# Kernel optimization log

Measured on AMD Instinct MI355X. Metric: run time of the kernel, lower is better.

The kernel has to match this reference:

```python
import jax, jax.numpy as jnp
import numpy as np

N_NODES = 50000
N_EDGES = 800000
N_GRAPHS = 64
IN_DIM = 128
HID = 64
HEADS = 4
LAT = 32
BN_EPS = 1e-5


def setup_inputs() -> dict:
    key = jax.random.key(0)
    ks = jax.random.split(key, 16)
    x = jax.random.normal(ks[0], (N_NODES, IN_DIM), jnp.float32)
    edge_index = jax.random.randint(ks[1], (2, N_EDGES), 0, N_NODES, dtype=jnp.int64)
    batch = jnp.sort(jax.random.randint(ks[2], (N_NODES,), 0, N_GRAPHS, dtype=jnp.int64))

    def lin(k, fan_in, shape):
        return (jax.random.normal(k, shape, jnp.float32) / np.sqrt(fan_in)).astype(jnp.float32)

    d = {"x": x, "edge_index": edge_index, "batch": batch}
    dims = [IN_DIM, HID, HID]
    i = 3
    for l, din in enumerate(dims):
        d[f"Wl{l}"] = lin(ks[i], din, (din, HEADS * HID)); i += 1
        d[f"Wr{l}"] = lin(ks[i], din, (din, HEADS * HID)); i += 1
        d[f"att{l}"] = lin(ks[i], HID, (HEADS, HID)); i += 1
        d[f"b{l}"] = jnp.zeros((HID,), jnp.float32)
    d["bn_gamma"] = jnp.ones((HID,), jnp.float32)
    d["bn_beta"] = jnp.zeros((HID,), jnp.float32)
    d["fc_W"] = lin(ks[i], HID, (LAT, HID)); i += 1
    d["fc_b"] = jnp.zeros((LAT,), jnp.float32)
    return d


def _gatv2_conv(x, Wl, Wr, att, b, src, dst):
    # PyG GATv2Conv, concat=False: mean over heads. src -> dst message flow.
    n = x.shape[0]
    H, D = att.shape
    xl = (x @ Wl).reshape(n, H, D)   # source-side transform
    xr = (x @ Wr).reshape(n, H, D)   # target-side transform
    e = jax.nn.leaky_relu(xl[src] + xr[dst], 0.2)        # [E, H, D]
    logits = jnp.einsum('ehd,hd->eh', e, att)            # [E, H]
    # segment softmax over incoming edges of each dst node
    m = jax.ops.segment_max(logits, dst, num_segments=n)
    p = jnp.exp(logits - m[dst])
    denom = jax.ops.segment_sum(p, dst, num_segments=n)
    alpha = p / (denom[dst] + 1e-16)                     # [E, H]
    out = jax.ops.segment_sum(alpha[..., None] * xl[src], dst, num_segments=n)  # [N, H, D]
    return out.mean(axis=1) + b


def reference(x, edge_index, batch, Wl0, Wr0, att0, b0, Wl1, Wr1, att1, b1,
              Wl2, Wr2, att2, b2, bn_gamma, bn_beta, fc_W, fc_b):
    src, dst = edge_index[0], edge_index[1]
    h = x
    for (Wl, Wr, att, b) in ((Wl0, Wr0, att0, b0), (Wl1, Wr1, att1, b1), (Wl2, Wr2, att2, b2)):
        h = _gatv2_conv(h, Wl, Wr, att, b, src, dst)
        h = jax.nn.leaky_relu(h, 0.1)
        # dropout omitted (deterministic reference / eval semantics)
    pooled = jax.ops.segment_sum(h, batch, num_segments=N_GRAPHS)  # [G, HID]
    mean = pooled.mean(axis=0)
    var = pooled.var(axis=0)  # biased variance, matches BN training normalization
    y = (pooled - mean) / jnp.sqrt(var + BN_EPS) * bn_gamma + bn_beta
    return y @ fc_W.T + fc_b
```

## Files before the change

kernel.cpp:

```cpp
#include <hip/hip_runtime.h>
#include <hip/hip_bf16.h>
#include <math.h>
#include <string.h>

#define N_NODES 50000
#define N_EDGES 800000
#define N_GRAPHS 64
#define IN_DIM 128
#define HID 64
#define HEADS 4
#define LAT 32
#define SCAN_BLOCKS ((N_NODES + 255) / 256)
#define ES_CAP 960000

typedef __attribute__((ext_vector_type(8))) short bf16x8;
typedef __attribute__((ext_vector_type(4))) float floatx4;
typedef __attribute__((ext_vector_type(2))) float f32x2;

__device__ inline unsigned short f2bf(float f) {
    unsigned u = __float_as_uint(f);
    return (unsigned short)((u + 0x7fffu + ((u >> 16) & 1u)) >> 16);
}

__device__ inline unsigned pkbf(float x, float y) {
    float2 f{x, y};
    __hip_bfloat162 h = __float22bfloat162_rn(f);
    unsigned u;
    memcpy(&u, &h, sizeof(u));
    return u;
}

__device__ inline f32x2 bfpair(unsigned u) {
    f32x2 r;
    r.x = __uint_as_float(u << 16);
    r.y = __uint_as_float(u & 0xffff0000u);
    return r;
}

__device__ inline float rowsum16(float x) {
    x += __int_as_float(__builtin_amdgcn_mov_dpp(__float_as_int(x), 0x128, 0xf, 0xf, false));
    x += __int_as_float(__builtin_amdgcn_mov_dpp(__float_as_int(x), 0x124, 0xf, 0xf, false));
    x += __int_as_float(__builtin_amdgcn_mov_dpp(__float_as_int(x), 0x122, 0xf, 0xf, false));
    x += __int_as_float(__builtin_amdgcn_mov_dpp(__float_as_int(x), 0x121, 0xf, 0xf, false));
    return x;
}

__global__ __launch_bounds__(256) void prep_kernel(
    const float* __restrict__ x, unsigned* __restrict__ xbf,
    const float* __restrict__ Wl0, const float* __restrict__ Wr0,
    const float* __restrict__ Wl1, const float* __restrict__ Wr1,
    const float* __restrict__ Wl2, const float* __restrict__ Wr2,
    unsigned short* __restrict__ B0, unsigned short* __restrict__ B1,
    unsigned short* __restrict__ B2,
    int* __restrict__ cnt, float* __restrict__ pooled, int* __restrict__ done,
    uint4* __restrict__ es4) {
    int b = blockIdx.x, t = threadIdx.x;
    if (b < 3072) {
        for (int i = b * 256 + t; i < N_NODES * IN_DIM / 2; i += 3072 * 256) {
            float2 v = reinterpret_cast<const float2*>(x)[i];
            xbf[i] = pkbf(v.x, v.y);
        }
    } else if (b < 3584) {
        int idx = (b - 3072) * 256 + t;
        const float *Wl, *Wr;
        unsigned short* B;
        int KC, local;
        if (idx < 65536)      { Wl = Wl0; Wr = Wr0; B = B0; KC = 4; local = idx; }
        else if (idx < 98304) { Wl = Wl1; Wr = Wr1; B = B1; KC = 2; local = idx - 65536; }
        else                  { Wl = Wl2; Wr = Wr2; B = B2; KC = 2; local = idx - 98304; }
        int j = local & 7;
        int lane = (local >> 3) & 63;
        int rem = local >> 9;
        int kc = rem % KC;
        int tile = rem / KC;
        int k = kc * 32 + (lane >> 4) * 8 + j;
        int tt = tile & 15;
        int n = (tt >> 2) * 64 + (lane & 15) * 4 + (tt & 3);
        const float* W = (tile < 16) ? Wl : Wr;
        B[local] = f2bf(W[k * 256 + n]);
    } else if (b < 3840) {
        int idx = (b - 3584) * 256 + t;
        if (idx < N_NODES) cnt[idx] = 0;
        if (idx < N_GRAPHS * HID) pooled[idx] = 0.f;
        if (idx == 0) *done = 0;
    } else {
        int idx = (b - 3840) * 256 + t;
        for (int i = idx; i < ES_CAP / 4; i += 65536)
            es4[i] = uint4{0, 0, 0, 0};
    }
}

__global__ __launch_bounds__(256) void deg_kernel(const int4* __restrict__ dsts4,
                                                  int* __restrict__ cnt, int E4) {
    int i = blockIdx.x * 256 + threadIdx.x;
    if (i < E4) {
        int4 d = dsts4[i];
        atomicAdd(&cnt[d.x], 1);
        atomicAdd(&cnt[d.y], 1);
        atomicAdd(&cnt[d.z], 1);
        atomicAdd(&cnt[d.w], 1);
    }
}

__global__ __launch_bounds__(256) void scan_kernel(const int* __restrict__ cnt,
                                                   int* __restrict__ offs,
                                                   int* __restrict__ sc,
                                                   int* __restrict__ agg) {
    __shared__ int buf[256];
    int b = blockIdx.x, t = threadIdx.x;
    int i = b * 256 + t;
    int v = (i < N_NODES) ? ((cnt[i] + 3) & ~3) : 0;
    buf[t] = v;
    __syncthreads();
    #pragma unroll
    for (int off = 1; off < 256; off <<= 1) {
        int tmp = (t >= off) ? buf[t - off] : 0;
        __syncthreads();
        buf[t] += tmp;
        __syncthreads();
    }
    int incl = buf[t];
    if (t == 255)
        __hip_atomic_store(&agg[b], buf[255] | 0x40000000,
                           __ATOMIC_RELEASE, __HIP_MEMORY_SCOPE_AGENT);
    int contrib = 0;
    if (t < b) {
        int vv;
        do {
            vv = __hip_atomic_load(&agg[t], __ATOMIC_ACQUIRE, __HIP_MEMORY_SCOPE_AGENT);
        } while (vv < 0 || !(vv & 0x40000000));
        contrib = vv & 0x3FFFFFFF;
    }
    __syncthreads();
    buf[t] = contrib;
    __syncthreads();
    for (int off = 128; off; off >>= 1) {
        if (t < off) buf[t] += buf[t + off];
        __syncthreads();
    }
    if (i < N_NODES) {
        offs[i] = buf[0] + incl - v;
        sc[i] = 0;
    }
}

__global__ __launch_bounds__(256) void scatter_kernel(const int4* __restrict__ srcs4,
                                                      const int4* __restrict__ dsts4,
                                                      const int* __restrict__ offs,
                                                      int* __restrict__ sc,
                                                      int* __restrict__ es, int E4) {
    int i = blockIdx.x * 256 + threadIdx.x;
    if (i < E4) {
        int4 s = srcs4[i];
        int4 d = dsts4[i];
        es[offs[d.x] + atomicAdd(&sc[d.x], 1)] = s.x;
        es[offs[d.y] + atomicAdd(&sc[d.y], 1)] = s.y;
        es[offs[d.z] + atomicAdd(&sc[d.z], 1)] = s.z;
        es[offs[d.w] + atomicAdd(&sc[d.w], 1)] = s.w;
    }
}

template <int K>
__global__ __launch_bounds__(512) void gemm_mfma_kernel(
    const unsigned short* __restrict__ Abf,
    const unsigned short* __restrict__ Bpk,
    unsigned* __restrict__ xlp_u,
    unsigned* __restrict__ xrp_u) {
    constexpr int KC = K / 32;
    constexpr int CHUNKS = 64 * K / 8;
    __shared__ short As[CHUNKS * 8];
    int br = blockIdx.x * 64;
    int t = threadIdx.x;

    for (int c = t; c < CHUNKS; c += 512) {
        int rt = c / (KC * 64);
        int rem = c % (KC * 64);
        int kc = rem >> 6;
        int quad = (rem >> 4) & 3, l16 = rem & 15;
        int row = br + rt * 16 + l16;
        if (row >= N_NODES) row = N_NODES - 1;
        *reinterpret_cast<uint4*>(&As[c * 8]) =
            *reinterpret_cast<const uint4*>(&Abf[(size_t)row * K + kc * 32 + quad * 8]);
    }
    __syncthreads();

    int wave = t >> 6, lane = t & 63;
    int quad = lane >> 4, l16 = lane & 15;
    int which = wave >> 2, g = wave & 3;

    bf16x8 afrag[4][KC];
    #pragma unroll
    for (int rt = 0; rt < 4; ++rt)
        #pragma unroll
        for (int kc = 0; kc < KC; ++kc)
            afrag[rt][kc] = *reinterpret_cast<const bf16x8*>(
                &As[(((rt * KC + kc) * 4 + quad) * 16 + l16) * 8]);

    floatx4 acc[4][4];
    #pragma unroll
    for (int rt = 0; rt < 4; ++rt)
        #pragma unroll
        for (int i = 0; i < 4; ++i) acc[rt][i] = floatx4{0.f, 0.f, 0.f, 0.f};

    #pragma unroll
    for (int i = 0; i < 4; ++i) {
        int T = which * 16 + g * 4 + i;
        #pragma unroll
        for (int kc = 0; kc < KC; ++kc) {
            bf16x8 bfr = *reinterpret_cast<const bf16x8*>(
                &Bpk[(size_t)((T * KC + kc) * 64 + lane) * 8]);
            #pragma unroll
            for (int rt = 0; rt < 4; ++rt)
                acc[rt][i] = __builtin_amdgcn_mfma_f32_16x16x32_bf16(
                    afrag[rt][kc], bfr, acc[rt][i], 0, 0, 0);
        }
    }

    unsigned* dst = which ? xrp_u : xlp_u;
    int dcol = g * 32 + l16 * 2;
    #pragma unroll
    for (int rt = 0; rt < 4; ++rt) {
        #pragma unroll
        for (int r = 0; r < 4; ++r) {
            int row = br + rt * 16 + quad * 4 + r;
            if (row >= N_NODES) continue;
            uint2 pk;
            pk.x = pkbf(acc[rt][0][r], acc[rt][1][r]);
            pk.y = pkbf(acc[rt][2][r], acc[rt][3][r]);
            *reinterpret_cast<uint2*>(&dst[(size_t)row * 128 + dcol]) = pk;
        }
    }
}

__global__ __launch_bounds__(256) void attn_kernel(const unsigned* __restrict__ xlp,
                                                   const unsigned* __restrict__ xrp,
                                                   const int* __restrict__ es,
                                                   const int* __restrict__ offs,
                                                   const int* __restrict__ deg,
                                                   const float4* __restrict__ att4,
                                                   const float4* __restrict__ bias4,
                                                   float* __restrict__ hout,
                                                   unsigned* __restrict__ hbf) {
    int node = blockIdx.x * 4 + (threadIdx.x >> 6);
    int lane = threadIdx.x & 63;
    int beg = offs[node];
    int end = beg + deg[node];
    uint2 xr2 = reinterpret_cast<const uint2*>(xrp)[(size_t)node * 64 + lane];
    f32x2 xrA = bfpair(xr2.x), xrB = bfpair(xr2.y);
    float4 at_t = att4[lane];
    f32x2 atA = {at_t.x, at_t.y}, atB = {at_t.z, at_t.w};
    const char* xbase = (const char*)xlp;
    int laneoff = lane << 3;

    float l = 0.f;
    f32x2 accA = {0.f, 0.f}, accB = {0.f, 0.f};

    auto edge_z = [&](uint2 v, f32x2& xa, f32x2& xb) -> float {
        xa = bfpair(v.x);
        xb = bfpair(v.y);
        f32x2 ea = xa + xrA;
        f32x2 eb = xb + xrB;
        ea = __builtin_elementwise_max(ea, ea * 0.2f);
        eb = __builtin_elementwise_max(eb, eb * 0.2f);
        f32x2 zz = ea * atA;
        zz += eb * atB;
        return zz.x + zz.y;
    };
    auto gather = [&](int s) -> uint2 {
        return *reinterpret_cast<const uint2*>(
            xbase + (((size_t)(unsigned)s) << 9) + laneoff);
    };

    for (int cb = beg; cb < end; cb += 4) {
        int4 s4 = *reinterpret_cast<const int4*>(&es[cb]);
        uint2 v0 = gather(s4.x);
        uint2 v1 = gather(s4.y);
        uint2 v2 = gather(s4.z);
        uint2 v3 = gather(s4.w);
        f32x2 xa0, xb0, xa1, xb1, xa2, xb2, xa3, xb3;
        float z0 = rowsum16(edge_z(v0, xa0, xb0));
        float z1 = rowsum16(edge_z(v1, xa1, xb1));
        float z2 = rowsum16(edge_z(v2, xa2, xb2));
        float z3 = rowsum16(edge_z(v3, xa3, xb3));
        float p0 = __expf(z0);
        float p1 = (cb + 1 < end) ? __expf(z1) : 0.f;
        float p2 = (cb + 2 < end) ? __expf(z2) : 0.f;
        float p3 = (cb + 3 < end) ? __expf(z3) : 0.f;
        accA += p0 * xa0 + p1 * xa1 + p2 * xa2 + p3 * xa3;
        accB += p0 * xb0 + p1 * xb1 + p2 * xb2 + p3 * xb3;
        l += (p0 + p1) + (p2 + p3);
    }

    float inv = 1.f / (l + 1e-16f);
    float a0 = accA.x * inv, a1 = accA.y * inv;
    float a2 = accB.x * inv, a3 = accB.y * inv;
    a0 += __shfl_xor(a0, 16); a0 += __shfl_xor(a0, 32);
    a1 += __shfl_xor(a1, 16); a1 += __shfl_xor(a1, 32);
    a2 += __shfl_xor(a2, 16); a2 += __shfl_xor(a2, 32);
    a3 += __shfl_xor(a3, 16); a3 += __shfl_xor(a3, 32);
    if (lane < 16) {
        float4 bv = bias4[lane];
        float4 o;
        o.x = 0.25f * a0 + bv.x; o.x = (o.x > 0.f) ? o.x : 0.1f * o.x;
        o.y = 0.25f * a1 + bv.y; o.y = (o.y > 0.f) ? o.y : 0.1f * o.y;
        o.z = 0.25f * a2 + bv.z; o.z = (o.z > 0.f) ? o.z : 0.1f * o.z;
        o.w = 0.25f * a3 + bv.w; o.w = (o.w > 0.f) ? o.w : 0.1f * o.w;
        if (hout)
            *reinterpret_cast<float4*>(&hout[(size_t)node * HID + lane * 4]) = o;
        if (hbf) {
            uint2 pk;
            pk.x = pkbf(o.x, o.y);
            pk.y = pkbf(o.z, o.w);
            *reinterpret_cast<uint2*>(&hbf[(size_t)node * 32 + lane * 2]) = pk;
        }
    }
}

__global__ __launch_bounds__(256) void pool_final_kernel(
    const float* __restrict__ hfin, const int* __restrict__ batch,
    float* __restrict__ pooled,
    const float* __restrict__ gamma, const float* __restrict__ beta,
    const float* __restrict__ fcW, const float* __restrict__ fcb,
    float* __restrict__ out, int* __restrict__ done) {
    int base = blockIdx.x * 256;
    int g = threadIdx.x >> 6, lane = threadIdx.x & 63;
    int lim = min(base + 256, N_NODES);
    int cur = -1;
    float s = 0.f;
    for (int i = base + g; i < lim; i += 4) {
        int b = batch[i];
        if (b != cur) {
            if (cur >= 0) atomicAdd(&pooled[cur * HID + lane], s);
            cur = b; s = 0.f;
        }
        s += hfin[(size_t)i * HID + lane];
    }
    if (cur >= 0) atomicAdd(&pooled[cur * HID + lane], s);

    __threadfence();
    __syncthreads();
    __shared__ int lastS;
    if (threadIdx.x == 0)
        lastS = (atomicAdd(done, 1) == (int)gridDim.x - 1);
    __syncthreads();
    if (!lastS) return;

    __shared__ float P[N_GRAPHS * HID];
    __shared__ float normS[N_GRAPHS * HID];
    __shared__ float meanS[HID], rstdS[HID];
    int t = threadIdx.x;
    for (int i = t; i < N_GRAPHS * HID; i += 256)
        P[i] = __hip_atomic_load(&pooled[i], __ATOMIC_RELAXED, __HIP_MEMORY_SCOPE_AGENT);
    __syncthreads();
    if (t < HID) {
        float s2 = 0.f;
        for (int g2 = 0; g2 < N_GRAPHS; ++g2) s2 += P[g2 * HID + t];
        float mean = s2 / (float)N_GRAPHS;
        float v = 0.f;
        for (int g2 = 0; g2 < N_GRAPHS; ++g2) {
            float dd = P[g2 * HID + t] - mean;
            v += dd * dd;
        }
        v /= (float)N_GRAPHS;
        meanS[t] = mean;
        rstdS[t] = rsqrtf(v + 1e-5f);
    }
    __syncthreads();
    for (int i = t; i < N_GRAPHS * HID; i += 256) {
        int d = i & 63;
        normS[i] = (P[i] - meanS[d]) * rstdS[d] * gamma[d] + beta[d];
    }
    __syncthreads();
    for (int i = t; i < N_GRAPHS * LAT; i += 256) {
        int g2 = i >> 5, lat = i & 31;
        float s2 = fcb[lat];
        for (int d = 0; d < HID; ++d) s2 += normS[g2 * HID + d] * fcW[lat * HID + d];
        out[i] = s2;
    }
}

extern "C" void kernel_launch(void* const* d_in, const int* in_sizes, int n_in,
                              void* d_out, int out_size, void* d_ws, size_t ws_size,
                              hipStream_t stream) {
    const float* x      = (const float*)d_in[0];
    const int*   ei     = (const int*)d_in[1];
    const int*   batch  = (const int*)d_in[2];
    const float* Wl[3]  = {(const float*)d_in[3], (const float*)d_in[7],  (const float*)d_in[11]};
    const float* Wr[3]  = {(const float*)d_in[4], (const float*)d_in[8],  (const float*)d_in[12]};
    const float* att[3] = {(const float*)d_in[5], (const float*)d_in[9],  (const float*)d_in[13]};
    const float* bia[3] = {(const float*)d_in[6], (const float*)d_in[10], (const float*)d_in[14]};
    const float* gamma  = (const float*)d_in[15];
    const float* beta   = (const float*)d_in[16];
    const float* fcW    = (const float*)d_in[17];
    const float* fcb    = (const float*)d_in[18];
    float* out = (float*)d_out;

    char* p = (char*)d_ws;
    auto alloc = [&](size_t bytes) {
        char* r = p;
        p += (bytes + 255) & ~(size_t)255;
        return r;
    };
    unsigned* xbf   = (unsigned*)alloc((size_t)N_NODES * IN_DIM * 2);
    unsigned* xlp   = (unsigned*)alloc((size_t)N_NODES * 256 * 2);
    unsigned* xrp   = (unsigned*)alloc((size_t)N_NODES * 256 * 2);
    unsigned* hbf0  = (unsigned*)alloc((size_t)N_NODES * HID * 2);
    unsigned* hbf1  = (unsigned*)alloc((size_t)N_NODES * HID * 2);
    unsigned short* Bpk0 = (unsigned short*)alloc(32 * 4 * 512 * 2);
    unsigned short* Bpk1 = (unsigned short*)alloc(32 * 2 * 512 * 2);
    unsigned short* Bpk2 = (unsigned short*)alloc(32 * 2 * 512 * 2);
    int*   es      = (int*)alloc((size_t)ES_CAP * 4);
    int*   offs    = (int*)alloc((size_t)N_NODES * 4);
    int*   cnt     = (int*)alloc((size_t)N_NODES * 4);
    int*   sc      = (int*)alloc((size_t)N_NODES * 4);
    int*   agg     = (int*)alloc((size_t)SCAN_BLOCKS * 4);
    int*   done    = (int*)alloc(256);
    float* pooled  = (float*)alloc((size_t)N_GRAPHS * HID * 4);
    float* hfin    = (float*)xbf;

    const int* srcs = ei;
    const int* dsts = ei + N_EDGES;

    prep_kernel<<<4096, 256, 0, stream>>>(x, xbf, Wl[0], Wr[0], Wl[1], Wr[1],
                                          Wl[2], Wr[2], Bpk0, Bpk1, Bpk2,
                                          cnt, pooled, done, (uint4*)es);
    int e4 = N_EDGES / 4;
    int eb4 = (e4 + 255) / 256;
    deg_kernel<<<eb4, 256, 0, stream>>>((const int4*)dsts, cnt, e4);
    scan_kernel<<<SCAN_BLOCKS, 256, 0, stream>>>(cnt, offs, sc, agg);
    scatter_kernel<<<eb4, 256, 0, stream>>>((const int4*)srcs, (const int4*)dsts,
                                            offs, sc, es, e4);

    int gb = (N_NODES + 63) / 64;
    gemm_mfma_kernel<IN_DIM><<<gb, 512, 0, stream>>>((const unsigned short*)xbf, Bpk0, xlp, xrp);
    attn_kernel<<<N_NODES / 4, 256, 0, stream>>>(xlp, xrp, es, offs, cnt,
                                                 (const float4*)att[0],
                                                 (const float4*)bia[0], nullptr, hbf0);
    gemm_mfma_kernel<HID><<<gb, 512, 0, stream>>>((const unsigned short*)hbf0, Bpk1, xlp, xrp);
    attn_kernel<<<N_NODES / 4, 256, 0, stream>>>(xlp, xrp, es, offs, cnt,
                                                 (const float4*)att[1],
                                                 (const float4*)bia[1], nullptr, hbf1);
    gemm_mfma_kernel<HID><<<gb, 512, 0, stream>>>((const unsigned short*)hbf1, Bpk2, xlp, xrp);
    attn_kernel<<<N_NODES / 4, 256, 0, stream>>>(xlp, xrp, es, offs, cnt,
                                                 (const float4*)att[2],
                                                 (const float4*)bia[2], hfin, nullptr);

    pool_final_kernel<<<SCAN_BLOCKS, 256, 0, stream>>>(hfin, batch, pooled,
                                                       gamma, beta, fcW, fcb,
                                                       out, done);
}
```

Before: 486.9 us.

## Fuse degree count into prep and CSR scatter into first GEMM launch

The degree-counting atomics now run as extra blocks of the prep kernel, with cnt zeroed by a memset beforehand. The edge scatter into CSR runs as extra blocks of the layer-0 GEMM launch. This removes two kernel launches and lets the independent atomic-heavy work overlap with the conversion and GEMM blocks. In exchange it adds a memset call, and the GEMM's shared-memory array is now sized for the largest case in all instantiations, which may lower occupancy for K=64.

Result: no change. 479.5 us (-1.5%).

```diff
diff --git a/kernel.cpp b/kernel.cpp
--- a/kernel.cpp
+++ b/kernel.cpp
@@ -53,7 +53,7 @@
     unsigned short* __restrict__ B0, unsigned short* __restrict__ B1,
     unsigned short* __restrict__ B2,
     int* __restrict__ cnt, float* __restrict__ pooled, int* __restrict__ done,
-    uint4* __restrict__ es4) {
+    uint4* __restrict__ es4, const int4* __restrict__ dsts4, int E4) {
     int b = blockIdx.x, t = threadIdx.x;
     if (b < 3072) {
         for (int i = b * 256 + t; i < N_NODES * IN_DIM / 2; i += 3072 * 256) {
@@ -80,25 +80,21 @@
         B[local] = f2bf(W[k * 256 + n]);
     } else if (b < 3840) {
         int idx = (b - 3584) * 256 + t;
-        if (idx < N_NODES) cnt[idx] = 0;
         if (idx < N_GRAPHS * HID) pooled[idx] = 0.f;
         if (idx == 0) *done = 0;
-    } else {
+    } else if (b < 4096) {
         int idx = (b - 3840) * 256 + t;
         for (int i = idx; i < ES_CAP / 4; i += 65536)
             es4[i] = uint4{0, 0, 0, 0};
-    }
-}
-
-__global__ __launch_bounds__(256) void deg_kernel(const int4* __restrict__ dsts4,
-                                                  int* __restrict__ cnt, int E4) {
-    int i = blockIdx.x * 256 + threadIdx.x;
-    if (i < E4) {
-        int4 d = dsts4[i];
-        atomicAdd(&cnt[d.x], 1);
-        atomicAdd(&cnt[d.y], 1);
-        atomicAdd(&cnt[d.z], 1);
-        atomicAdd(&cnt[d.w], 1);
+    } else {
+        int i = (b - 4096) * 256 + t;
+        if (i < E4) {
+            int4 d = dsts4[i];
+            atomicAdd(&cnt[d.x], 1);
+            atomicAdd(&cnt[d.y], 1);
+            atomicAdd(&cnt[d.z], 1);
+            atomicAdd(&cnt[d.w], 1);
+        }
     }
 }
 
@@ -144,33 +140,16 @@
     }
 }
 
-__global__ __launch_bounds__(256) void scatter_kernel(const int4* __restrict__ srcs4,
-                                                      const int4* __restrict__ dsts4,
-                                                      const int* __restrict__ offs,
-                                                      int* __restrict__ sc,
-                                                      int* __restrict__ es, int E4) {
-    int i = blockIdx.x * 256 + threadIdx.x;
-    if (i < E4) {
-        int4 s = srcs4[i];
-        int4 d = dsts4[i];
-        es[offs[d.x] + atomicAdd(&sc[d.x], 1)] = s.x;
-        es[offs[d.y] + atomicAdd(&sc[d.y], 1)] = s.y;
-        es[offs[d.z] + atomicAdd(&sc[d.z], 1)] = s.z;
-        es[offs[d.w] + atomicAdd(&sc[d.w], 1)] = s.w;
-    }
-}
-
 template <int K>
-__global__ __launch_bounds__(512) void gemm_mfma_kernel(
+__device__ __forceinline__ void gemm_body(
     const unsigned short* __restrict__ Abf,
     const unsigned short* __restrict__ Bpk,
     unsigned* __restrict__ xlp_u,
-    unsigned* __restrict__ xrp_u) {
+    unsigned* __restrict__ xrp_u, int blk, int t) {
     constexpr int KC = K / 32;
     constexpr int CHUNKS = 64 * K / 8;
-    __shared__ short As[CHUNKS * 8];
-    int br = blockIdx.x * 64;
-    int t = threadIdx.x;
+    __shared__ short As[1024 * 8];
+    int br = blk * 64;
 
     for (int c = t; c < CHUNKS; c += 512) {
         int rt = c / (KC * 64);
@@ -230,6 +209,35 @@
             *reinterpret_cast<uint2*>(&dst[(size_t)row * 128 + dcol]) = pk;
         }
     }
+}
+
+__global__ __launch_bounds__(512) void gemm0_scatter_kernel(
+    const unsigned short* __restrict__ Abf,
+    const unsigned short* __restrict__ Bpk,
+    unsigned* __restrict__ xlp_u, unsigned* __restrict__ xrp_u,
+    const int4* __restrict__ srcs4, const int4* __restrict__ dsts4,
+    const int* __restrict__ offs, int* __restrict__ sc,
+    int* __restrict__ es, int E4, int GB) {
+    if ((int)blockIdx.x < GB) {
+        gemm_body<IN_DIM>(Abf, Bpk, xlp_u, xrp_u, blockIdx.x, threadIdx.x);
+    } else {
+        int i = (blockIdx.x - GB) * 512 + threadIdx.x;
+        if (i < E4) {
+            int4 s = srcs4[i];
+            int4 d = dsts4[i];
+            es[offs[d.x] + atomicAdd(&sc[d.x], 1)] = s.x;
+            es[offs[d.y] + atomicAdd(&sc[d.y], 1)] = s.y;
+            es[offs[d.z] + atomicAdd(&sc[d.z], 1)] = s.z;
+            es[offs[d.w] + atomicAdd(&sc[d.w], 1)] = s.w;
+        }
+    }
+}
+
+__global__ __launch_bounds__(512) void gemm_kernel64(
+    const unsigned short* __restrict__ Abf,
+    const unsigned short* __restrict__ Bpk,
+    unsigned* __restrict__ xlp_u, unsigned* __restrict__ xrp_u) {
+    gemm_body<HID>(Abf, Bpk, xlp_u, xrp_u, blockIdx.x, threadIdx.x);
 }
 
 __global__ __launch_bounds__(256) void attn_kernel(const unsigned* __restrict__ xlp,
@@ -420,27 +428,31 @@
 
     const int* srcs = ei;
     const int* dsts = ei + N_EDGES;
-
-    prep_kernel<<<4096, 256, 0, stream>>>(x, xbf, Wl[0], Wr[0], Wl[1], Wr[1],
-                                          Wl[2], Wr[2], Bpk0, Bpk1, Bpk2,
-                                          cnt, pooled, done, (uint4*)es);
     int e4 = N_EDGES / 4;
-    int eb4 = (e4 + 255) / 256;
-    deg_kernel<<<eb4, 256, 0, stream>>>((const int4*)dsts, cnt, e4);
+
+    hipMemsetAsync(cnt, 0, (size_t)N_NODES * 4, stream);
+
+    int degb = (e4 + 255) / 256;
+    prep_kernel<<<4096 + degb, 256, 0, stream>>>(x, xbf, Wl[0], Wr[0], Wl[1], Wr[1],
+                                                 Wl[2], Wr[2], Bpk0, Bpk1, Bpk2,
+                                                 cnt, pooled, done, (uint4*)es,
+                                                 (const int4*)dsts, e4);
     scan_kernel<<<SCAN_BLOCKS, 256, 0, stream>>>(cnt, offs, sc, agg);
-    scatter_kernel<<<eb4, 256, 0, stream>>>((const int4*)srcs, (const int4*)dsts,
-                                            offs, sc, es, e4);
 
     int gb = (N_NODES + 63) / 64;
-    gemm_mfma_kernel<IN_DIM><<<gb, 512, 0, stream>>>((const unsigned short*)xbf, Bpk0, xlp, xrp);
+    int sb = (e4 + 511) / 512;
+    gemm0_scatter_kernel<<<gb + sb, 512, 0, stream>>>(
+        (const unsigned short*)xbf, Bpk0, xlp, xrp,
+        (const int4*)srcs, (const int4*)dsts, offs, sc, es, e4, gb);
+
     attn_kernel<<<N_NODES / 4, 256, 0, stream>>>(xlp, xrp, es, offs, cnt,
                                                  (const float4*)att[0],
                                                  (const float4*)bia[0], nullptr, hbf0);
-    gemm_mfma_kernel<HID><<<gb, 512, 0, stream>>>((const unsigned short*)hbf0, Bpk1, xlp, xrp);
+    gemm_kernel64<<<gb, 512, 0, stream>>>((const unsigned short*)hbf0, Bpk1, xlp, xrp);
     attn_kernel<<<N_NODES / 4, 256, 0, stream>>>(xlp, xrp, es, offs, cnt,
                                                  (const float4*)att[1],
                                                  (const float4*)bia[1], nullptr, hbf1);
-    gemm_mfma_kernel<HID><<<gb, 512, 0, stream>>>((const unsigned short*)hbf1, Bpk2, xlp, xrp);
+    gemm_kernel64<<<gb, 512, 0, stream>>>((const unsigned short*)hbf1, Bpk2, xlp, xrp);
     attn_kernel<<<N_NODES / 4, 256, 0, stream>>>(xlp, xrp, es, offs, cnt,
                                                  (const float4*)att[2],
                                                  (const float4*)bia[2], hfin, nullptr);
```
